# Kernel tuning notes

Measured on AMD Instinct MI355X. Metric: run time of the kernel, lower is better.

## Reference

```python
import jax, jax.numpy as jnp
import numpy as np


def _silu(x):
    return x * jax.nn.sigmoid(x)


def _ln(x, w, b, eps=1e-5):
    mu = x.mean(-1, keepdims=True)
    xc = x - mu
    var = (xc * xc).mean(-1, keepdims=True)
    return xc * jax.lax.rsqrt(var + eps) * w + b


def _segsum(a):
    # a: (..., Q) -> (..., Q, Q) lower-triangular cumulative segment sums
    Q = a.shape[-1]
    cs = jnp.cumsum(a, axis=-1)
    ss = cs[..., :, None] - cs[..., None, :]
    mask = jnp.tril(jnp.ones((Q, Q), dtype=bool))
    return jnp.where(mask, ss, -jnp.inf)


def _ssd(x, A, Bm, Cm, chunk=64):
    # Mamba2 SSD dual (chunked) form. x:(b,l,h,p) pre-scaled by dt, A:(b,l,h)=dt*A, Bm/Cm:(b,l,n)
    b, l, h, p = x.shape
    c = l // chunk
    x = x.reshape(b, c, chunk, h, p)
    A = A.reshape(b, c, chunk, h).transpose(0, 3, 1, 2)          # (b,h,c,q)
    Bm = Bm.reshape(b, c, chunk, -1)
    Cm = Cm.reshape(b, c, chunk, -1)
    Acs = jnp.cumsum(A, axis=-1)                                  # (b,h,c,q)
    Lmat = jnp.exp(_segsum(A))                                    # (b,h,c,q,q)
    Yd = jnp.einsum('bcln,bcsn,bhcls,bcshp->bclhp', Cm, Bm, Lmat, x)
    dec = jnp.exp(Acs[..., -1:] - Acs)                            # (b,h,c,q)
    states = jnp.einsum('bcln,bhcl,bclhp->bchpn', Bm, dec, x)     # (b,c,h,p,n)
    cdec = jnp.exp(Acs[..., -1]).transpose(2, 0, 1)               # (c,b,h)
    st = states.transpose(1, 0, 2, 3, 4)                          # (c,b,h,p,n)

    def step(carry, inp):
        s, d = inp
        return carry * d[..., None, None] + s, carry

    _, prev = jax.lax.scan(step, jnp.zeros_like(st[0]), (st, cdec))
    prev = prev.transpose(1, 0, 2, 3, 4)                          # (b,c,h,p,n)
    Yo = jnp.einsum('bcln,bchpn,bhcl->bclhp', Cm, prev, jnp.exp(Acs))
    return (Yd + Yo).reshape(b, l, h, p)


def _mamba(x, in_w, in_b, conv_w, conv_b, A_log, D, dt_bias, rms_w, out_w, headdim, d_state):
    b, l, _ = x.shape
    nh = A_log.shape[0]
    di = nh * headdim
    zxbcdt = x @ in_w.T + in_b
    z = zxbcdt[..., :di]
    xBC = zxbcdt[..., di:2 * di + 2 * d_state]
    dt = jax.nn.softplus(zxbcdt[..., -nh:] + dt_bias)             # (b,l,nh)
    K = conv_w.shape[-1]
    xp = jnp.pad(xBC, ((0, 0), (K - 1, 0), (0, 0)))               # causal depthwise conv
    xBC = sum(xp[:, k:k + l, :] * conv_w[:, k] for k in range(K))
    xBC = _silu(xBC + conv_b)
    xs = xBC[..., :di].reshape(b, l, nh, headdim)
    Bm = xBC[..., di:di + d_state]
    Cm = xBC[..., di + d_state:]
    A = -jnp.exp(A_log)
    y = _ssd(xs * dt[..., None], dt * A, Bm, Cm)
    y = y + D[None, None, :, None] * xs
    y = y.reshape(b, l, di) * _silu(z)                            # gated RMSNorm
    y = y * jax.lax.rsqrt(jnp.mean(y * y, -1, keepdims=True) + 1e-5) * rms_w
    return y @ out_w.T


def setup_inputs() -> dict:
    key = jax.random.key(0)
    ks = iter(jax.random.split(key, 64))

    def nrm(shape, s):
        return jax.random.normal(next(ks), shape, jnp.float32) * s

    d = {}
    d['x'] = jax.random.normal(next(ks), (4, 128, 64, 64), jnp.float32)
    d['seed_tok_w'] = nrm((8, 128), 0.08)
    d['seed_tok_b'] = jnp.zeros((8,), jnp.float32)
    d['seed_detok_w'] = nrm((128, 8), 0.3)
    d['seed_detok_b'] = jnp.zeros((128,), jnp.float32)
    d['sm_in_w'] = nrm((66, 8), 0.3)
    d['sm_in_b'] = jnp.zeros((66,), jnp.float32)
    d['sm_conv_w'] = nrm((48, 3), 0.3)
    d['sm_conv_b'] = jnp.zeros((48,), jnp.float32)
    d['sm_A_log'] = jnp.log(jnp.arange(1, 3, dtype=jnp.float32))
    d['sm_D'] = jnp.ones((2,), jnp.float32)
    d['sm_dt_bias'] = jnp.full((2,), -4.0, jnp.float32)
    d['sm_rms_w'] = jnp.ones((16,), jnp.float32)
    d['sm_out_w'] = nrm((8, 16), 0.2)
    d['cm_in_w'] = nrm((2, 196, 16), 0.2)
    d['cm_in_b'] = jnp.zeros((2, 196), jnp.float32)
    d['cm_conv_w'] = nrm((2, 160, 3), 0.3)
    d['cm_conv_b'] = jnp.zeros((2, 160), jnp.float32)
    d['cm_A_log'] = jnp.tile(jnp.log(jnp.arange(1, 5, dtype=jnp.float32)), (2, 1))
    d['cm_D'] = jnp.ones((2, 4), jnp.float32)
    d['cm_dt_bias'] = jnp.full((2, 4), -4.0, jnp.float32)
    d['cm_rms_w'] = jnp.ones((2, 32), jnp.float32)
    d['cm_out_w'] = nrm((2, 16, 32), 0.15)
    d['cross_W'] = jnp.eye(8, dtype=jnp.float32) + 0.01 * jax.random.normal(next(ks), (8, 8), jnp.float32)
    d['norm1_w'] = jnp.ones((128,), jnp.float32)
    d['norm1_b'] = jnp.zeros((128,), jnp.float32)
    d['norm2_w'] = jnp.ones((128,), jnp.float32)
    d['norm2_b'] = jnp.zeros((128,), jnp.float32)
    d['fc1_w'] = nrm((256, 128), 0.08)
    d['fc1_b'] = jnp.zeros((256,), jnp.float32)
    d['dw_w'] = nrm((256, 1, 3, 3), 0.2)
    d['dw_b'] = jnp.zeros((256,), jnp.float32)
    d['fc2_w'] = nrm((128, 256), 0.06)
    d['fc2_b'] = jnp.zeros((128,), jnp.float32)
    d['skip_scale'] = jnp.ones((1,), jnp.float32)
    return d


def reference(x, seed_tok_w, seed_tok_b, seed_detok_w, seed_detok_b,
              sm_in_w, sm_in_b, sm_conv_w, sm_conv_b, sm_A_log, sm_D, sm_dt_bias, sm_rms_w, sm_out_w,
              cm_in_w, cm_in_b, cm_conv_w, cm_conv_b, cm_A_log, cm_D, cm_dt_bias, cm_rms_w, cm_out_w,
              cross_W, norm1_w, norm1_b, norm2_w, norm2_b,
              fc1_w, fc1_b, dw_w, dw_b, fc2_w, fc2_b, skip_scale):
    B, C, H, W = x.shape
    L = H * W
    # --- GlobalSeed ---
    g = jnp.einsum('bchw,gc->bghw', x, seed_tok_w) + seed_tok_b[None, :, None, None]
    gf = g.reshape(B, -1, L).transpose(0, 2, 1)                   # (B,L,G)
    gf = _mamba(gf, sm_in_w, sm_in_b, sm_conv_w, sm_conv_b, sm_A_log, sm_D,
                sm_dt_bias, sm_rms_w, sm_out_w, 8, 16) + gf
    det = jnp.einsum('blg,cg->blc', gf, seed_detok_w) + seed_detok_b
    seed = x + det.transpose(0, 2, 1).reshape(B, C, H, W)
    # --- split-channel cascaded SSD (shared weights across splits) ---
    xn = _ln(x.reshape(B, C, L).transpose(0, 2, 1), norm1_w, norm1_b)   # (B,L,C)
    S = cross_W.shape[0]
    xs = jnp.stack(jnp.split(xn, S, axis=-1))                     # (S,B,L,C/S)

    def cascade(xi):
        for i in range(cm_in_w.shape[0]):
            xi = _mamba(xi, cm_in_w[i], cm_in_b[i], cm_conv_w[i], cm_conv_b[i],
                        cm_A_log[i], cm_D[i], cm_dt_bias[i], cm_rms_w[i], cm_out_w[i], 8, 64)
        return xi

    ys = jax.vmap(cascade)(xs) + xs * skip_scale
    # --- SubCrossToken mixing ---
    gm = ys.mean(axis=2)                                          # (S,B,Cs)
    wsm = jax.nn.softmax(cross_W, axis=1)
    gmix = jnp.einsum('qbc,qp->pbc', gm, wsm)
    ys = ys + gmix[:, :, None, :]
    out = ys.transpose(1, 2, 0, 3).reshape(B, L, -1)
    out = _ln(out, norm2_w, norm2_b)
    out = out.transpose(0, 2, 1).reshape(B, C, H, W) + seed
    # --- ConvFFN ---
    h1 = jnp.einsum('bchw,oc->bohw', out, fc1_w) + fc1_b[None, :, None, None]
    dw = jax.lax.conv_general_dilated(h1, dw_w, (1, 1), 'SAME',
                                      feature_group_count=h1.shape[1],
                                      dimension_numbers=('NCHW', 'OIHW', 'NCHW'))
    h2 = jax.nn.gelu(dw + dw_b[None, :, None, None])
    ffn = jnp.einsum('bohw,co->bchw', h2, fc2_w) + fc2_b[None, :, None, None]
    return out + ffn
```

## Files before the change

### kernel.cpp

```cpp
#include <hip/hip_runtime.h>
#include <math.h>

#define B_ 4
#define CCH 128
#define HH 64
#define WW 64
#define LL 4096
#define NCHK 64

__device__ __forceinline__ float siluf(float x) { return x / (1.f + __expf(-x)); }
__device__ __forceinline__ float softplusf(float x) { return (x > 20.f) ? x : log1pf(__expf(x)); }
__device__ __forceinline__ int swz(int n, int l) {
  return (n << 6) + ((((l >> 2) ^ ((n >> 2) & 15)) << 2) | (l & 3));
}

__global__ __launch_bounds__(256) void k_seedtok(const float* __restrict__ x,
    const float* __restrict__ w, const float* __restrict__ bias, float* __restrict__ gf)
{
  __shared__ float sw[8*128];
  int tid = threadIdx.x;
  for (int i = tid; i < 1024; i += 256) sw[i] = w[i];
  __syncthreads();
  int idx = blockIdx.x * 256 + tid;
  int b = idx / LL, l = idx % LL;
  const float* xp = x + (size_t)b*CCH*LL + l;
  float acc[8];
#pragma unroll
  for (int g = 0; g < 8; ++g) acc[g] = bias[g];
  for (int c = 0; c < CCH; ++c) {
    float xv = xp[(size_t)c*LL];
#pragma unroll
    for (int g = 0; g < 8; ++g) acc[g] += xv * sw[g*128 + c];
  }
  float* o = gf + (size_t)idx*8;
#pragma unroll
  for (int g = 0; g < 8; ++g) o[g] = acc[g];
}

template<int DIN, int NZ, int NDS, int NDT>
__global__ __launch_bounds__(256) void k_inproj(
    const float* __restrict__ src,
    const float* __restrict__ in_w, const float* __restrict__ in_b,
    const float* __restrict__ conv_w, const float* __restrict__ conv_b,
    const float* __restrict__ dt_bias,
    float* __restrict__ zb, float* __restrict__ dtb,
    float* __restrict__ xsb, float* __restrict__ Bb, float* __restrict__ Cb)
{
  constexpr int NXBC = NZ + 2*NDS;
  constexpr int NTOT = 2*NZ + 2*NDS + NDT;
  constexpr int NZQ  = NZ/4;
  constexpr int NDSQ = NDS/4;
  constexpr int XP   = DIN + 1;
  __shared__ float xt[66*XP];
  __shared__ float wl[NTOT*DIN];
  __shared__ float cwl[NXBC*3];
  __shared__ float cbl[NXBC];
  __shared__ float ibl[NTOT];
  __shared__ float dts[64*NDT];
  int tid = threadIdx.x;
  int seq = blockIdx.x >> 6;
  int l0  = (blockIdx.x & 63) << 6;
  for (int i = tid; i < NTOT*DIN; i += 256) wl[i] = in_w[i];
  for (int i = tid; i < NXBC*3; i += 256) cwl[i] = conv_w[i];
  for (int i = tid; i < NXBC; i += 256) cbl[i] = conv_b[i];
  for (int i = tid; i < NTOT; i += 256) ibl[i] = in_b[i];
  for (int i = tid; i < 66*DIN; i += 256) {
    int r = i / DIN, d = i % DIN;
    int l = l0 - 2 + r;
    xt[r*XP + d] = (l >= 0) ? src[((size_t)seq*LL + l)*DIN + d] : 0.f;
  }
  __syncthreads();
  int l = tid & 63, w = tid >> 6;
  float xr0[DIN], xr1[DIN], xr2[DIN];
#pragma unroll
  for (int d = 0; d < DIN; ++d) {
    xr0[d] = xt[l*XP + d];
    xr1[d] = xt[(l+1)*XP + d];
    xr2[d] = xt[(l+2)*XP + d];
  }
  size_t gl = (size_t)seq*LL + l0 + l;
  int tok = l0 + l;
  {
    float zv[NZQ];
#pragma unroll
    for (int j = 0; j < NZQ; ++j) {
      int row = w*NZQ + j;
      const float* wr = &wl[row*DIN];
      float acc = ibl[row];
#pragma unroll
      for (int d = 0; d < DIN; ++d) acc += xr2[d]*wr[d];
      zv[j] = acc;
    }
#pragma unroll
    for (int g = 0; g < NZQ/4; ++g)
      *(float4*)&zb[gl*NZ + w*NZQ + 4*g] = make_float4(zv[4*g], zv[4*g+1], zv[4*g+2], zv[4*g+3]);
  }
  if (w < NDT) {
    int row = NTOT - NDT + w;
    const float* wr = &wl[row*DIN];
    float acc = ibl[row] + dt_bias[w];
#pragma unroll
    for (int d = 0; d < DIN; ++d) acc += xr2[d]*wr[d];
    dts[l*NDT + w] = softplusf(acc);
  }
  float v0ok = (tok >= 2) ? 1.f : 0.f;
  float v1ok = (tok >= 1) ? 1.f : 0.f;
  {
    float xv[NZQ];
#pragma unroll
    for (int j = 0; j < NZQ; ++j) {
      int ch = w*NZQ + j;
      int row = NZ + ch;
      const float* wr = &wl[row*DIN];
      float p0 = 0.f, p1 = 0.f, p2 = 0.f;
#pragma unroll
      for (int d = 0; d < DIN; ++d) {
        float ww = wr[d];
        p0 += xr0[d]*ww; p1 += xr1[d]*ww; p2 += xr2[d]*ww;
      }
      float ib = ibl[row];
      float conv = cbl[ch] + (p0+ib)*v0ok*cwl[ch*3+0] + (p1+ib)*v1ok*cwl[ch*3+1] + (p2+ib)*cwl[ch*3+2];
      xv[j] = siluf(conv);
    }
#pragma unroll
    for (int g = 0; g < NZQ/4; ++g)
      *(float4*)&xsb[gl*NZ + w*NZQ + 4*g] = make_float4(xv[4*g], xv[4*g+1], xv[4*g+2], xv[4*g+3]);
  }
  {
    float bv[NDSQ];
#pragma unroll
    for (int j = 0; j < NDSQ; ++j) {
      int ch = NZ + w*NDSQ + j;
      int row = NZ + ch;
      const float* wr = &wl[row*DIN];
      float p0 = 0.f, p1 = 0.f, p2 = 0.f;
#pragma unroll
      for (int d = 0; d < DIN; ++d) {
        float ww = wr[d];
        p0 += xr0[d]*ww; p1 += xr1[d]*ww; p2 += xr2[d]*ww;
      }
      float ib = ibl[row];
      float conv = cbl[ch] + (p0+ib)*v0ok*cwl[ch*3+0] + (p1+ib)*v1ok*cwl[ch*3+1] + (p2+ib)*cwl[ch*3+2];
      bv[j] = siluf(conv);
    }
#pragma unroll
    for (int g = 0; g < NDSQ/4; ++g)
      *(float4*)&Bb[gl*NDS + w*NDSQ + 4*g] = make_float4(bv[4*g], bv[4*g+1], bv[4*g+2], bv[4*g+3]);
  }
  {
    float cv[NDSQ];
#pragma unroll
    for (int j = 0; j < NDSQ; ++j) {
      int ch = NZ + NDS + w*NDSQ + j;
      int row = NZ + ch;
      const float* wr = &wl[row*DIN];
      float p0 = 0.f, p1 = 0.f, p2 = 0.f;
#pragma unroll
      for (int d = 0; d < DIN; ++d) {
        float ww = wr[d];
        p0 += xr0[d]*ww; p1 += xr1[d]*ww; p2 += xr2[d]*ww;
      }
      float ib = ibl[row];
      float conv = cbl[ch] + (p0+ib)*v0ok*cwl[ch*3+0] + (p1+ib)*v1ok*cwl[ch*3+1] + (p2+ib)*cwl[ch*3+2];
      cv[j] = siluf(conv);
    }
#pragma unroll
    for (int g = 0; g < NDSQ/4; ++g)
      *(float4*)&Cb[gl*NDS + w*NDSQ + 4*g] = make_float4(cv[4*g], cv[4*g+1], cv[4*g+2], cv[4*g+3]);
  }
  __syncthreads();
  if (tid < 64) {
    if constexpr (NDT == 4) {
      float4 v = *(float4*)&dts[tid*4];
      *(float4*)&dtb[((size_t)seq*LL + l0 + tid)*4] = v;
    } else {
      float2 v = *(float2*)&dts[tid*NDT];
      *(float2*)&dtb[((size_t)seq*LL + l0 + tid)*NDT] = v;
    }
  }
}

template<int DS, int NH>
__global__ __launch_bounds__(256) void k_ssd1(
    const float* __restrict__ xs, const float* __restrict__ dtb,
    const float* __restrict__ Bb, const float* __restrict__ Cb,
    const float* __restrict__ A_log,
    float* __restrict__ ybuf, float* __restrict__ states,
    float* __restrict__ cdec, float* __restrict__ acsOut)
{
  constexpr int DI = NH*8;
  constexpr int NG = DS/4;
  __shared__ __align__(16) float BtBl[DS*64];
  __shared__ __align__(16) float CtGt[64*64];
  __shared__ __align__(16) float xde[NH*64*8];
  __shared__ __align__(16) float xde2[NH*64*8];
  int tid = threadIdx.x;
  int cid = blockIdx.x & 63;
  int seq = blockIdx.x >> 6;
  int l0  = cid << 6;
  for (int i = tid; i < 16*DS; i += 256) {
    int ng = i % NG, l = i / NG;
    size_t g = ((size_t)seq*LL + l0 + l)*DS + 4*ng;
    float4 bv = *(const float4*)&Bb[g];
    float4 cv = *(const float4*)&Cb[g];
    BtBl[swz(4*ng+0, l)] = bv.x; BtBl[swz(4*ng+1, l)] = bv.y;
    BtBl[swz(4*ng+2, l)] = bv.z; BtBl[swz(4*ng+3, l)] = bv.w;
    CtGt[swz(4*ng+0, l)] = cv.x; CtGt[swz(4*ng+1, l)] = cv.y;
    CtGt[swz(4*ng+2, l)] = cv.z; CtGt[swz(4*ng+3, l)] = cv.w;
  }
  __syncthreads();
  int lt = (tid >> 4) << 2, st = (tid & 15) << 2;
  float acc[4][4] = {};
#pragma unroll 4
  for (int n = 0; n < DS; ++n) {
    float4 cv = *(const float4*)&CtGt[swz(n, lt)];
    float4 bv = *(const float4*)&BtBl[swz(n, st)];
    float cc[4] = {cv.x, cv.y, cv.z, cv.w};
    float bb[4] = {bv.x, bv.y, bv.z, bv.w};
#pragma unroll
    for (int i2 = 0; i2 < 4; ++i2)
#pragma unroll
      for (int j2 = 0; j2 < 4; ++j2)
        acc[i2][j2] += cc[i2]*bb[j2];
  }
  __syncthreads();
#pragma unroll
  for (int j = 0; j < 4; ++j) {
    float4 gv = make_float4(acc[0][j], acc[1][j], acc[2][j], acc[3][j]);
    *(float4*)&CtGt[swz(st + j, lt)] = gv;
  }
  for (int i = tid; i < 16*DS; i += 256) {
    int ng = i % NG, l = i / NG;
    float4 bv = *(const float4*)&Bb[((size_t)seq*LL + l0 + l)*DS + 4*ng];
    *(float4*)&BtBl[l*DS + 4*ng] = bv;
  }
  __syncthreads();
  int w = tid >> 6, lane = tid & 63;
  if (w < NH) {
    int h = w;
    float dt_l = dtb[((size_t)seq*LL + l0 + lane)*NH + h];
    float Aval = -__expf(A_log[h]);
    float v = dt_l * Aval;
#pragma unroll
    for (int off = 1; off < 64; off <<= 1) {
      float t = __shfl_up(v, off, 64);
      if (lane >= off) v += t;
    }
    float acs_l = v;
    float m = __shfl(v, 31, 64);
    float acsLast = __shfl(v, 63, 64);
    float el = __expf(fminf(acs_l - m, 60.f));
    float fl = __expf(fminf(m - acs_l, 60.f));
    float dec = __expf(acsLast - acs_l);
    const float* xp = &xs[((size_t)seq*LL + l0 + lane)*DI + h*8];
    float4 x0 = *(const float4*)xp, x1 = *(const float4*)(xp + 4);
    float s1 = dt_l*fl, s2 = dt_l*dec;
    float* xe = &xde[(h*64 + lane)*8];
    float* xf = &xde2[(h*64 + lane)*8];
    *(float4*)xe     = make_float4(x0.x*s1, x0.y*s1, x0.z*s1, x0.w*s1);
    *(float4*)(xe+4) = make_float4(x1.x*s1, x1.y*s1, x1.z*s1, x1.w*s1);
// ... 102 lines not shown
    const float* __restrict__ ybuf, const float* __restrict__ zbuf,
    const float* __restrict__ rms_w, const float* __restrict__ out_w,
    float* __restrict__ dst, int resMode, const float* __restrict__ res,
    const float* __restrict__ skipPtr)
{
  __shared__ float ow[DOUT*DI];
  __shared__ float rw[DI];
  int tid = threadIdx.x;
  for (int i = tid; i < DOUT*DI; i += 256) ow[i] = out_w[i];
  for (int i = tid; i < DI; i += 256) rw[i] = rms_w[i];
  __syncthreads();
  size_t idx = (size_t)blockIdx.x*256 + tid;
  float y[DI];
  const float* yp = ybuf + idx*DI;
  const float* zp = zbuf + idx*DI;
  float ss = 0.f;
#pragma unroll
  for (int i = 0; i < DI; ++i) {
    float z = zp[i];
    float g = yp[i] * (z / (1.f + __expf(-z)));
    y[i] = g; ss += g*g;
  }
  float r = rsqrtf(ss*(1.f/DI) + 1e-5f);
#pragma unroll
  for (int i = 0; i < DI; ++i) y[i] *= r*rw[i];
  const float* rp = nullptr; float skip = 1.f;
  int seq = (int)(idx / LL), l = (int)(idx % LL);
  if (resMode == 1) rp = res + idx*DOUT;
  else if (resMode == 2) {
    int s = seq / B_, b = seq % B_;
    rp = res + ((size_t)b*LL + l)*CCH + s*DOUT;
    skip = skipPtr[0];
  }
  float* dp = dst + idx*DOUT;
#pragma unroll
  for (int o = 0; o < DOUT; ++o) {
    float acc = 0.f;
#pragma unroll
    for (int i = 0; i < DI; ++i) acc += y[i]*ow[o*DI + i];
    if (rp) acc += skip * rp[o];
    dp[o] = acc;
  }
}

__global__ __launch_bounds__(256) void k_detseed(const float* __restrict__ x,
    const float* __restrict__ gf2, const float* __restrict__ dw,
    const float* __restrict__ db, float* __restrict__ seed)
{
  size_t idx = (size_t)blockIdx.x*256 + threadIdx.x;
  int l = (int)(idx % LL); size_t t = idx / LL; int c = (int)(t % CCH); int b = (int)(t / CCH);
  const float* g = gf2 + ((size_t)b*LL + l)*8;
  float acc = db[c];
#pragma unroll
  for (int i = 0; i < 8; ++i) acc += g[i]*dw[c*8 + i];
  seed[idx] = x[idx] + acc;
}

__global__ __launch_bounds__(256) void k_ln1(const float* __restrict__ x,
    const float* __restrict__ w, const float* __restrict__ bb, float* __restrict__ xn)
{
  __shared__ float tile[128*65];
  __shared__ float mu[64], rs[64];
  int tid = threadIdx.x;
  int b = blockIdx.x >> 6;
  int l0 = (blockIdx.x & 63) << 6;
  for (int i = tid; i < 8192; i += 256) {
    int l = i & 63, c = i >> 6;
    tile[c*65 + l] = x[((size_t)b*CCH + c)*LL + l0 + l];
  }
  __syncthreads();
  if (tid < 64) {
    float s = 0.f;
    for (int c = 0; c < CCH; ++c) s += tile[c*65 + tid];
    float m = s * (1.f/CCH);
    float v = 0.f;
    for (int c = 0; c < CCH; ++c) { float d = tile[c*65 + tid] - m; v += d*d; }
    mu[tid] = m; rs[tid] = rsqrtf(v*(1.f/CCH) + 1e-5f);
  }
  __syncthreads();
  for (int i = tid; i < 8192; i += 256) {
    int c = i & 127, l = i >> 7;
    xn[((size_t)b*LL + l0 + l)*CCH + c] = (tile[c*65 + l] - mu[l])*rs[l]*w[c] + bb[c];
  }
}

__global__ __launch_bounds__(256) void k_split(const float* __restrict__ xn, float* __restrict__ X)
{
  size_t idx = (size_t)blockIdx.x*256 + threadIdx.x;
  int c = (int)(idx & 15); size_t t = idx >> 4; int l = (int)(t % LL); int seq = (int)(t / LL);
  int s = seq / B_, b = seq % B_;
  X[idx] = xn[((size_t)b*LL + l)*CCH + s*16 + c];
}

__global__ __launch_bounds__(256) void k_gm(const float* __restrict__ ys, float* __restrict__ gm)
{
  __shared__ float red[256];
  int tid = threadIdx.x;
  int seq = blockIdx.x;
  int c = tid & 15, lane = tid >> 4;
  float s = 0.f;
  for (int l = lane; l < LL; l += 16) s += ys[((size_t)seq*LL + l)*16 + c];
  red[tid] = s;
  __syncthreads();
  if (tid < 16) {
    float t = 0.f;
    for (int g = 0; g < 16; ++g) t += red[g*16 + tid];
    gm[(size_t)seq*16 + tid] = t * (1.f/LL);
  }
}

__global__ __launch_bounds__(256) void k_mix(const float* __restrict__ gm,
    const float* __restrict__ crossW, float* __restrict__ gmix)
{
  __shared__ float wsm[64];
  int tid = threadIdx.x;
  if (tid < 8) {
    float mx = -1e30f;
    for (int p = 0; p < 8; ++p) mx = fmaxf(mx, crossW[tid*8 + p]);
    float e[8]; float s = 0.f;
    for (int p = 0; p < 8; ++p) { e[p] = __expf(crossW[tid*8 + p] - mx); s += e[p]; }
    for (int p = 0; p < 8; ++p) wsm[tid*8 + p] = e[p] / s;
  }
  __syncthreads();
  for (int i = tid; i < 512; i += 256) {
    int c = i & 15; int bb = (i >> 4) & 3; int p = i >> 6;
    float acc = 0.f;
    for (int q = 0; q < 8; ++q) acc += gm[((size_t)(q*B_ + bb))*16 + c] * wsm[q*8 + p];
    gmix[((size_t)(p*B_ + bb))*16 + c] = acc;
  }
}

__global__ __launch_bounds__(256) void k_out2(const float* __restrict__ ys,
    const float* __restrict__ gmix, const float* __restrict__ w, const float* __restrict__ bb,
    const float* __restrict__ seed, float* __restrict__ outb)
{
  __shared__ float tile[128*65];
  __shared__ float mu[64], rs[64];
  int tid = threadIdx.x;
  int b = blockIdx.x >> 6;
  int l0 = (blockIdx.x & 63) << 6;
  for (int i = tid; i < 8192; i += 256) {
    int c = i & 15; int l = (i >> 4) & 63; int s = i >> 10;
    int seq = s*B_ + b;
    tile[(s*16 + c)*65 + l] = ys[((size_t)seq*LL + l0 + l)*16 + c] + gmix[(size_t)seq*16 + c];
  }
  __syncthreads();
  if (tid < 64) {
    float sm = 0.f;
    for (int c = 0; c < 128; ++c) sm += tile[c*65 + tid];
    float m = sm * (1.f/128.f);
    float v = 0.f;
    for (int c = 0; c < 128; ++c) { float d = tile[c*65 + tid] - m; v += d*d; }
    mu[tid] = m; rs[tid] = rsqrtf(v*(1.f/128.f) + 1e-5f);
  }
  __syncthreads();
  for (int i = tid; i < 8192; i += 256) {
    int l = i & 63, c = i >> 6;
    size_t gi = ((size_t)b*CCH + c)*LL + l0 + l;
    outb[gi] = (tile[c*65 + l] - mu[l])*rs[l]*w[c] + bb[c] + seed[gi];
  }
}

__global__ __launch_bounds__(256) void k_fc1(const float* __restrict__ src,
    const float* __restrict__ w, const float* __restrict__ bias, float* __restrict__ dst)
{
  constexpr int WP = 129;
  __shared__ float st[128*64];
  __shared__ float wt[64*WP];
  int tid = threadIdx.x;
  int blk = blockIdx.x;
  int ot = blk & 3;
  int lt = (blk >> 2) & 63;
  int b  = blk >> 8;
  int l0 = lt << 6, o0 = ot << 6;
// ... 81 lines not shown
      int l = i & 63, o = i >> 6;
      st[o*64 + l] = h2[((size_t)b*256 + ko + o)*LL + l0 + l];
    }
    __syncthreads();
#pragma unroll 4
    for (int o = 0; o < 128; ++o) {
      float4 sv = *(float4*)&st[o*64 + l4];
      float w0 = wt[(c2+0)*WP + ko + o];
      float w1 = wt[(c2+1)*WP + ko + o];
      a0[0] += w0*sv.x; a0[1] += w0*sv.y; a0[2] += w0*sv.z; a0[3] += w0*sv.w;
      a1[0] += w1*sv.x; a1[1] += w1*sv.y; a1[2] += w1*sv.z; a1[3] += w1*sv.w;
    }
  }
  float* rows[2] = {a0, a1};
#pragma unroll
  for (int j = 0; j < 2; ++j) {
    int c = c0 + c2 + j;
    float bi = bias[c];
    size_t gi = ((size_t)b*CCH + c)*LL + l0 + l4;
    float4 rv = *(const float4*)&resid[gi];
    float* a = rows[j];
    *(float4*)&dst[gi] = make_float4(a[0]+bi+rv.x, a[1]+bi+rv.y, a[2]+bi+rv.z, a[3]+bi+rv.w);
  }
}

extern "C" void kernel_launch(void* const* d_in, const int* in_sizes, int n_in,
                              void* d_out, int out_size, void* d_ws, size_t ws_size,
                              hipStream_t stream) {
  (void)in_sizes; (void)n_in; (void)out_size; (void)ws_size;
  const float* x        = (const float*)d_in[0];
  const float* tok_w    = (const float*)d_in[1];
  const float* tok_b    = (const float*)d_in[2];
  const float* detok_w  = (const float*)d_in[3];
  const float* detok_b  = (const float*)d_in[4];
  const float* sm_in_w  = (const float*)d_in[5];
  const float* sm_in_b  = (const float*)d_in[6];
  const float* sm_conv_w= (const float*)d_in[7];
  const float* sm_conv_b= (const float*)d_in[8];
  const float* sm_A_log = (const float*)d_in[9];
  const float* sm_D     = (const float*)d_in[10];
  const float* sm_dt_b  = (const float*)d_in[11];
  const float* sm_rms_w = (const float*)d_in[12];
  const float* sm_out_w = (const float*)d_in[13];
  const float* cm_in_w  = (const float*)d_in[14];
  const float* cm_in_b  = (const float*)d_in[15];
  const float* cm_conv_w= (const float*)d_in[16];
  const float* cm_conv_b= (const float*)d_in[17];
  const float* cm_A_log = (const float*)d_in[18];
  const float* cm_D     = (const float*)d_in[19];
  const float* cm_dt_b  = (const float*)d_in[20];
  const float* cm_rms_w = (const float*)d_in[21];
  const float* cm_out_w = (const float*)d_in[22];
  const float* cross_W  = (const float*)d_in[23];
  const float* n1w      = (const float*)d_in[24];
  const float* n1b      = (const float*)d_in[25];
  const float* n2w      = (const float*)d_in[26];
  const float* n2b      = (const float*)d_in[27];
  const float* fc1w     = (const float*)d_in[28];
  const float* fc1b     = (const float*)d_in[29];
  const float* dww      = (const float*)d_in[30];
  const float* dwb      = (const float*)d_in[31];
  const float* fc2w     = (const float*)d_in[32];
  const float* fc2b     = (const float*)d_in[33];
  const float* skp      = (const float*)d_in[34];
  float* ws  = (float*)d_ws;
  float* out = (float*)d_out;

  const size_t SEED = 0;
  const size_t XN   = 2097152;
  const size_t YS   = 4194304;
  const size_t OUTB = 6291456;
  const size_t GM   = 8388608;
  const size_t GMIX = 8389120;
  const size_t SCR  = 8389632;
  const size_t CZ   = SCR;
  const size_t CDT  = CZ   + 4194304;
  const size_t CXS  = CDT  + 524288;
  const size_t CBF  = CXS  + 4194304;
  const size_t CCF  = CBF  + 8388608;
  const size_t CACS = CCF  + 8388608;
  const size_t CST  = CACS + 2097152;
  const size_t CCD  = CST  + 4194304;
  const size_t CY   = CCD  + 8192;
  const size_t XA   = CY   + 4194304;
  const size_t XB   = XA   + 2097152;
  const size_t SGF  = SCR;
  const size_t SZ   = SCR + 131072;
  const size_t SDT  = SCR + 393216;
  const size_t SXS  = SCR + 425984;
  const size_t SB   = SCR + 688128;
  const size_t SC   = SCR + 950272;
  const size_t SACS = SCR + 1212416;
  const size_t SST  = SCR + 1245184;
  const size_t SCD  = SCR + 1310720;
  const size_t SY   = SCR + 1311232;
  const size_t SOUT = SCR + 1573376;
  const size_t H1 = SCR;
  const size_t H2 = SCR + 4194304;

  k_seedtok<<<64, 256, 0, stream>>>(x, tok_w, tok_b, ws + SGF);
  k_inproj<8,16,16,2><<<B_*64, 256, 0, stream>>>(ws + SGF, sm_in_w, sm_in_b, sm_conv_w,
      sm_conv_b, sm_dt_b, ws + SZ, ws + SDT, ws + SXS, ws + SB, ws + SC);
  k_ssd1<16,2><<<B_*NCHK, 256, 0, stream>>>(ws + SXS, ws + SDT, ws + SB, ws + SC,
      sm_A_log, ws + SY, ws + SST, ws + SCD, ws + SACS);
  k_scan<<<B_*2, 128, 0, stream>>>(ws + SST, ws + SCD, 128);
  k_ssd_yo<16,2><<<B_*NCHK, 256, 0, stream>>>(ws + SY, ws + SC, ws + SST, ws + SACS, sm_D, ws + SXS);
  k_gate<16,8><<<B_*LL/256, 256, 0, stream>>>(ws + SY, ws + SZ, sm_rms_w, sm_out_w,
      ws + SOUT, 1, ws + SGF, skp);
  k_detseed<<<B_*CCH*LL/256, 256, 0, stream>>>(x, ws + SOUT, detok_w, detok_b, ws + SEED);

  k_ln1<<<B_*64, 256, 0, stream>>>(x, n1w, n1b, ws + XN);
  k_split<<<32*LL*16/256, 256, 0, stream>>>(ws + XN, ws + XA);

  k_inproj<16,32,64,4><<<32*64, 256, 0, stream>>>(ws + XA, cm_in_w, cm_in_b, cm_conv_w,
      cm_conv_b, cm_dt_b, ws + CZ, ws + CDT, ws + CXS, ws + CBF, ws + CCF);
  k_ssd1<64,4><<<32*NCHK, 256, 0, stream>>>(ws + CXS, ws + CDT, ws + CBF, ws + CCF,
      cm_A_log, ws + CY, ws + CST, ws + CCD, ws + CACS);
  k_scan<<<32*4, 512, 0, stream>>>(ws + CST, ws + CCD, 512);
  k_ssd_yo<64,4><<<32*NCHK, 256, 0, stream>>>(ws + CY, ws + CCF, ws + CST, ws + CACS, cm_D, ws + CXS);
  k_gate<32,16><<<32*LL/256, 256, 0, stream>>>(ws + CY, ws + CZ, cm_rms_w, cm_out_w,
      ws + XB, 0, nullptr, skp);

  k_inproj<16,32,64,4><<<32*64, 256, 0, stream>>>(ws + XB, cm_in_w + 3136, cm_in_b + 196,
      cm_conv_w + 480, cm_conv_b + 160, cm_dt_b + 4, ws + CZ, ws + CDT, ws + CXS, ws + CBF, ws + CCF);
  k_ssd1<64,4><<<32*NCHK, 256, 0, stream>>>(ws + CXS, ws + CDT, ws + CBF, ws + CCF,
      cm_A_log + 4, ws + CY, ws + CST, ws + CCD, ws + CACS);
  k_scan<<<32*4, 512, 0, stream>>>(ws + CST, ws + CCD, 512);
  k_ssd_yo<64,4><<<32*NCHK, 256, 0, stream>>>(ws + CY, ws + CCF, ws + CST, ws + CACS, cm_D + 4, ws + CXS);
  k_gate<32,16><<<32*LL/256, 256, 0, stream>>>(ws + CY, ws + CZ, cm_rms_w + 32, cm_out_w + 512,
      ws + YS, 2, ws + XN, skp);

  k_gm<<<32, 256, 0, stream>>>(ws + YS, ws + GM);
  k_mix<<<1, 256, 0, stream>>>(ws + GM, cross_W, ws + GMIX);
  k_out2<<<B_*64, 256, 0, stream>>>(ws + YS, ws + GMIX, n2w, n2b, ws + SEED, ws + OUTB);

  k_fc1<<<B_*64*4, 256, 0, stream>>>(ws + OUTB, fc1w, fc1b, ws + H1);
  k_dw<<<B_*256*LL/256, 256, 0, stream>>>(ws + H1, dww, dwb, ws + H2);
  k_fc2<<<B_*64*4, 256, 0, stream>>>(ws + H2, fc2w, fc2b, ws + OUTB, out);
}
```

Before: 654.1 us.

## Register-tile in_proj over 4 tokens per thread and fuse split into it

Reworks the in_proj/conv kernel so each thread computes 4 consecutive tokens for a group of channels, keeping 6 input rows and one weight row in registers. Inputs are read straight from global memory as float4 instead of through a shared tile. Outputs are staged in padded shared tiles and written back with coalesced float4 stores. A srcMode flag lets the first cascade stage read the LN output through strides, which removes the separate k_split kernel and its round trip through global memory. The cost is higher register pressure from xr[6][DIN] and more shared memory for the output tiles, which may lower occupancy.

Measured after the change: 725.5 us. 1.11x slower.

```diff
diff --git a/kernel.cpp b/kernel.cpp
--- a/kernel.cpp
+++ b/kernel.cpp
@@ -39,7 +39,7 @@
 
 template<int DIN, int NZ, int NDS, int NDT>
 __global__ __launch_bounds__(256) void k_inproj(
-    const float* __restrict__ src,
+    const float* __restrict__ src, int srcMode,
     const float* __restrict__ in_w, const float* __restrict__ in_b,
     const float* __restrict__ conv_w, const float* __restrict__ conv_b,
     const float* __restrict__ dt_bias,
@@ -48,15 +48,20 @@
 {
   constexpr int NXBC = NZ + 2*NDS;
   constexpr int NTOT = 2*NZ + 2*NDS + NDT;
-  constexpr int NZQ  = NZ/4;
-  constexpr int NDSQ = NDS/4;
-  constexpr int XP   = DIN + 1;
-  __shared__ float xt[66*XP];
+  constexpr int ZR = NZ/16;
+  constexpr int BR = NDS/16;
+  constexpr int PZ = NZ + 1;
+  constexpr int PB = NDS + 1;
+  constexpr int PD = NDT + 1;
   __shared__ float wl[NTOT*DIN];
   __shared__ float cwl[NXBC*3];
   __shared__ float cbl[NXBC];
   __shared__ float ibl[NTOT];
-  __shared__ float dts[64*NDT];
+  __shared__ float zt[64*PZ];
+  __shared__ float xt2[64*PZ];
+  __shared__ float Bt[64*PB];
+  __shared__ float Ct[64*PB];
+  __shared__ float dtt[64*PD];
   int tid = threadIdx.x;
   int seq = blockIdx.x >> 6;
   int l0  = (blockIdx.x & 63) << 6;
@@ -64,118 +69,164 @@
   for (int i = tid; i < NXBC*3; i += 256) cwl[i] = conv_w[i];
   for (int i = tid; i < NXBC; i += 256) cbl[i] = conv_b[i];
   for (int i = tid; i < NTOT; i += 256) ibl[i] = in_b[i];
-  for (int i = tid; i < 66*DIN; i += 256) {
-    int r = i / DIN, d = i % DIN;
-    int l = l0 - 2 + r;
-    xt[r*XP + d] = (l >= 0) ? src[((size_t)seq*LL + l)*DIN + d] : 0.f;
-  }
-  __syncthreads();
-  int l = tid & 63, w = tid >> 6;
-  float xr0[DIN], xr1[DIN], xr2[DIN];
-#pragma unroll
-  for (int d = 0; d < DIN; ++d) {
-    xr0[d] = xt[l*XP + d];
-    xr1[d] = xt[(l+1)*XP + d];
-    xr2[d] = xt[(l+2)*XP + d];
-  }
-  size_t gl = (size_t)seq*LL + l0 + l;
-  int tok = l0 + l;
-  {
-    float zv[NZQ];
-#pragma unroll
-    for (int j = 0; j < NZQ; ++j) {
-      int row = w*NZQ + j;
-      const float* wr = &wl[row*DIN];
-      float acc = ibl[row];
-#pragma unroll
-      for (int d = 0; d < DIN; ++d) acc += xr2[d]*wr[d];
-      zv[j] = acc;
-    }
-#pragma unroll
-    for (int g = 0; g < NZQ/4; ++g)
-      *(float4*)&zb[gl*NZ + w*NZQ + 4*g] = make_float4(zv[4*g], zv[4*g+1], zv[4*g+2], zv[4*g+3]);
-  }
-  if (w < NDT) {
-    int row = NTOT - NDT + w;
-    const float* wr = &wl[row*DIN];
-    float acc = ibl[row] + dt_bias[w];
-#pragma unroll
-    for (int d = 0; d < DIN; ++d) acc += xr2[d]*wr[d];
-    dts[l*NDT + w] = softplusf(acc);
-  }
-  float v0ok = (tok >= 2) ? 1.f : 0.f;
-  float v1ok = (tok >= 1) ? 1.f : 0.f;
-  {
-    float xv[NZQ];
-#pragma unroll
-    for (int j = 0; j < NZQ; ++j) {
-      int ch = w*NZQ + j;
-      int row = NZ + ch;
-      const float* wr = &wl[row*DIN];
-      float p0 = 0.f, p1 = 0.f, p2 = 0.f;
+  __syncthreads();
+  int tg = tid & 15, cg = tid >> 4;
+  const float* sp; int sstr;
+  if (srcMode == 0) { sp = src + (size_t)seq*LL*DIN; sstr = DIN; }
+  else { sp = src + (size_t)(seq & 3)*LL*CCH + (seq >> 2)*16; sstr = CCH; }
+  float xr[6][DIN];
+#pragma unroll
+  for (int jj = 0; jj < 6; ++jj) {
+    int t = l0 + 4*tg - 2 + jj;
+    if (t >= 0) {
+      const float* p = sp + (size_t)t*sstr;
+#pragma unroll
+      for (int k = 0; k < DIN/4; ++k) {
+        float4 v = *(const float4*)(p + 4*k);
+        xr[jj][4*k+0]=v.x; xr[jj][4*k+1]=v.y; xr[jj][4*k+2]=v.z; xr[jj][4*k+3]=v.w;
+      }
+    } else {
+#pragma unroll
+      for (int d = 0; d < DIN; ++d) xr[jj][d] = 0.f;
+    }
+  }
+  float mk0[4], mk1[4];
+#pragma unroll
+  for (int j = 0; j < 4; ++j) {
+    int t = l0 + 4*tg + j;
+    mk0[j] = (t >= 2) ? 1.f : 0.f;
+    mk1[j] = (t >= 1) ? 1.f : 0.f;
+  }
+  float w[DIN];
+#pragma unroll
+  for (int r = 0; r < ZR; ++r) {
+    int row = cg*ZR + r;
+#pragma unroll
+    for (int k = 0; k < DIN/4; ++k) {
+      float4 v = *(const float4*)&wl[row*DIN + 4*k];
+      w[4*k]=v.x; w[4*k+1]=v.y; w[4*k+2]=v.z; w[4*k+3]=v.w;
+    }
+    float ib = ibl[row];
+#pragma unroll
+    for (int j = 0; j < 4; ++j) {
+      float acc = ib;
+#pragma unroll
+      for (int d = 0; d < DIN; ++d) acc += xr[2+j][d]*w[d];
+      zt[(4*tg+j)*PZ + row] = acc;
+    }
+  }
+  if (cg < NDT) {
+    int row = NTOT - NDT + cg;
+#pragma unroll
+    for (int k = 0; k < DIN/4; ++k) {
+      float4 v = *(const float4*)&wl[row*DIN + 4*k];
+      w[4*k]=v.x; w[4*k+1]=v.y; w[4*k+2]=v.z; w[4*k+3]=v.w;
+    }
+    float ib = ibl[row] + dt_bias[cg];
+#pragma unroll
+    for (int j = 0; j < 4; ++j) {
+      float acc = ib;
+#pragma unroll
+      for (int d = 0; d < DIN; ++d) acc += xr[2+j][d]*w[d];
+      dtt[(4*tg+j)*PD + cg] = softplusf(acc);
+    }
+  }
+#pragma unroll
+  for (int r = 0; r < ZR; ++r) {
+    int ch = cg*ZR + r;
+    int row = NZ + ch;
+#pragma unroll
+    for (int k = 0; k < DIN/4; ++k) {
+      float4 v = *(const float4*)&wl[row*DIN + 4*k];
+      w[4*k]=v.x; w[4*k+1]=v.y; w[4*k+2]=v.z; w[4*k+3]=v.w;
+    }
+    float ib = ibl[row];
+    float cw0 = cwl[ch*3+0], cw1 = cwl[ch*3+1], cw2 = cwl[ch*3+2], cb = cbl[ch];
+#pragma unroll
+    for (int j = 0; j < 4; ++j) {
+      float p0=0.f, p1=0.f, p2=0.f;
 #pragma unroll
       for (int d = 0; d < DIN; ++d) {
-        float ww = wr[d];
-        p0 += xr0[d]*ww; p1 += xr1[d]*ww; p2 += xr2[d]*ww;
+        p0 += xr[j][d]*w[d];
+        p1 += xr[j+1][d]*w[d];
+        p2 += xr[j+2][d]*w[d];
       }
-      float ib = ibl[row];
-      float conv = cbl[ch] + (p0+ib)*v0ok*cwl[ch*3+0] + (p1+ib)*v1ok*cwl[ch*3+1] + (p2+ib)*cwl[ch*3+2];
-      xv[j] = siluf(conv);
-    }
-#pragma unroll
-    for (int g = 0; g < NZQ/4; ++g)
-      *(float4*)&xsb[gl*NZ + w*NZQ + 4*g] = make_float4(xv[4*g], xv[4*g+1], xv[4*g+2], xv[4*g+3]);
-  }
-  {
-    float bv[NDSQ];
-#pragma unroll
-    for (int j = 0; j < NDSQ; ++j) {
-      int ch = NZ + w*NDSQ + j;
-      int row = NZ + ch;
-      const float* wr = &wl[row*DIN];
-      float p0 = 0.f, p1 = 0.f, p2 = 0.f;
+      float conv = cb + (p0+ib)*mk0[j]*cw0 + (p1+ib)*mk1[j]*cw1 + (p2+ib)*cw2;
+      xt2[(4*tg+j)*PZ + ch] = siluf(conv);
+    }
+  }
+#pragma unroll
+  for (int r = 0; r < BR; ++r) {
+    int chl = cg*BR + r;
+    int ch = NZ + chl;
+    int row = NZ + ch;
+#pragma unroll
+    for (int k = 0; k < DIN/4; ++k) {
+      float4 v = *(const float4*)&wl[row*DIN + 4*k];
+      w[4*k]=v.x; w[4*k+1]=v.y; w[4*k+2]=v.z; w[4*k+3]=v.w;
+    }
+    float ib = ibl[row];
+    float cw0 = cwl[ch*3+0], cw1 = cwl[ch*3+1], cw2 = cwl[ch*3+2], cb = cbl[ch];
+#pragma unroll
+    for (int j = 0; j < 4; ++j) {
+      float p0=0.f, p1=0.f, p2=0.f;
 #pragma unroll
       for (int d = 0; d < DIN; ++d) {
-        float ww = wr[d];
-        p0 += xr0[d]*ww; p1 += xr1[d]*ww; p2 += xr2[d]*ww;
+        p0 += xr[j][d]*w[d];
+        p1 += xr[j+1][d]*w[d];
+        p2 += xr[j+2][d]*w[d];
       }
-      float ib = ibl[row];
-      float conv = cbl[ch] + (p0+ib)*v0ok*cwl[ch*3+0] + (p1+ib)*v1ok*cwl[ch*3+1] + (p2+ib)*cwl[ch*3+2];
-      bv[j] = siluf(conv);
-    }
-#pragma unroll
-    for (int g = 0; g < NDSQ/4; ++g)
-      *(float4*)&Bb[gl*NDS + w*NDSQ + 4*g] = make_float4(bv[4*g], bv[4*g+1], bv[4*g+2], bv[4*g+3]);
-  }
-  {
-    float cv[NDSQ];
-#pragma unroll
-    for (int j = 0; j < NDSQ; ++j) {
-      int ch = NZ + NDS + w*NDSQ + j;
-      int row = NZ + ch;
-      const float* wr = &wl[row*DIN];
-      float p0 = 0.f, p1 = 0.f, p2 = 0.f;
+      float conv = cb + (p0+ib)*mk0[j]*cw0 + (p1+ib)*mk1[j]*cw1 + (p2+ib)*cw2;
+      Bt[(4*tg+j)*PB + chl] = siluf(conv);
+    }
+  }
+#pragma unroll
+  for (int r = 0; r < BR; ++r) {
+    int chl = cg*BR + r;
+    int ch = NZ + NDS + chl;
+    int row = NZ + ch;
+#pragma unroll
+    for (int k = 0; k < DIN/4; ++k) {
+      float4 v = *(const float4*)&wl[row*DIN + 4*k];
+      w[4*k]=v.x; w[4*k+1]=v.y; w[4*k+2]=v.z; w[4*k+3]=v.w;
+    }
+    float ib = ibl[row];
+    float cw0 = cwl[ch*3+0], cw1 = cwl[ch*3+1], cw2 = cwl[ch*3+2], cb = cbl[ch];
+#pragma unroll
+    for (int j = 0; j < 4; ++j) {
+      float p0=0.f, p1=0.f, p2=0.f;
 #pragma unroll
       for (int d = 0; d < DIN; ++d) {
-        float ww = wr[d];
-        p0 += xr0[d]*ww; p1 += xr1[d]*ww; p2 += xr2[d]*ww;
+        p0 += xr[j][d]*w[d];
+        p1 += xr[j+1][d]*w[d];
+        p2 += xr[j+2][d]*w[d];
       }
-      float ib = ibl[row];
-      float conv = cbl[ch] + (p0+ib)*v0ok*cwl[ch*3+0] + (p1+ib)*v1ok*cwl[ch*3+1] + (p2+ib)*cwl[ch*3+2];
-      cv[j] = siluf(conv);
-    }
-#pragma unroll
-    for (int g = 0; g < NDSQ/4; ++g)
-      *(float4*)&Cb[gl*NDS + w*NDSQ + 4*g] = make_float4(cv[4*g], cv[4*g+1], cv[4*g+2], cv[4*g+3]);
-  }
-  __syncthreads();
+      float conv = cb + (p0+ib)*mk0[j]*cw0 + (p1+ib)*mk1[j]*cw1 + (p2+ib)*cw2;
+      Ct[(4*tg+j)*PB + chl] = siluf(conv);
+    }
+  }
+  __syncthreads();
+  size_t gb = (size_t)seq*LL + l0;
+  for (int i = tid; i < 64*(NZ/4); i += 256) {
+    int l = i / (NZ/4), k = (i % (NZ/4))*4;
+    *(float4*)&zb[(gb+l)*NZ + k] =
+        make_float4(zt[l*PZ+k], zt[l*PZ+k+1], zt[l*PZ+k+2], zt[l*PZ+k+3]);
+    *(float4*)&xsb[(gb+l)*NZ + k] =
+        make_float4(xt2[l*PZ+k], xt2[l*PZ+k+1], xt2[l*PZ+k+2], xt2[l*PZ+k+3]);
+  }
+  for (int i = tid; i < 64*(NDS/4); i += 256) {
+    int l = i / (NDS/4), k = (i % (NDS/4))*4;
+    *(float4*)&Bb[(gb+l)*NDS + k] =
+        make_float4(Bt[l*PB+k], Bt[l*PB+k+1], Bt[l*PB+k+2], Bt[l*PB+k+3]);
+    *(float4*)&Cb[(gb+l)*NDS + k] =
+        make_float4(Ct[l*PB+k], Ct[l*PB+k+1], Ct[l*PB+k+2], Ct[l*PB+k+3]);
+  }
   if (tid < 64) {
     if constexpr (NDT == 4) {
-      float4 v = *(float4*)&dts[tid*4];
-      *(float4*)&dtb[((size_t)seq*LL + l0 + tid)*4] = v;
+      *(float4*)&dtb[(gb+tid)*4] =
+          make_float4(dtt[tid*PD], dtt[tid*PD+1], dtt[tid*PD+2], dtt[tid*PD+3]);
     } else {
-      float2 v = *(float2*)&dts[tid*NDT];
-      *(float2*)&dtb[((size_t)seq*LL + l0 + tid)*NDT] = v;
+      *(float2*)&dtb[(gb+tid)*NDT] = make_float2(dtt[tid*PD], dtt[tid*PD+1]);
     }
   }
 }
@@ -444,14 +495,6 @@
     int c = i & 127, l = i >> 7;
     xn[((size_t)b*LL + l0 + l)*CCH + c] = (tile[c*65 + l] - mu[l])*rs[l]*w[c] + bb[c];
   }
-}
-
-__global__ __launch_bounds__(256) void k_split(const float* __restrict__ xn, float* __restrict__ X)
-{
-  size_t idx = (size_t)blockIdx.x*256 + threadIdx.x;
-  int c = (int)(idx & 15); size_t t = idx >> 4; int l = (int)(t % LL); int seq = (int)(t / LL);
-  int s = seq / B_, b = seq % B_;
-  X[idx] = xn[((size_t)b*LL + l)*CCH + s*16 + c];
 }
 
 __global__ __launch_bounds__(256) void k_gm(const float* __restrict__ ys, float* __restrict__ gm)
@@ -716,7 +759,7 @@
   const size_t H2 = SCR + 4194304;
 
   k_seedtok<<<64, 256, 0, stream>>>(x, tok_w, tok_b, ws + SGF);
-  k_inproj<8,16,16,2><<<B_*64, 256, 0, stream>>>(ws + SGF, sm_in_w, sm_in_b, sm_conv_w,
+  k_inproj<8,16,16,2><<<B_*64, 256, 0, stream>>>(ws + SGF, 0, sm_in_w, sm_in_b, sm_conv_w,
       sm_conv_b, sm_dt_b, ws + SZ, ws + SDT, ws + SXS, ws + SB, ws + SC);
   k_ssd1<16,2><<<B_*NCHK, 256, 0, stream>>>(ws + SXS, ws + SDT, ws + SB, ws + SC,
       sm_A_log, ws + SY, ws + SST, ws + SCD, ws + SACS);
@@ -727,9 +770,8 @@
   k_detseed<<<B_*CCH*LL/256, 256, 0, stream>>>(x, ws + SOUT, detok_w, detok_b, ws + SEED);
 
   k_ln1<<<B_*64, 256, 0, stream>>>(x, n1w, n1b, ws + XN);
-  k_split<<<32*LL*16/256, 256, 0, stream>>>(ws + XN, ws + XA);
-
-  k_inproj<16,32,64,4><<<32*64, 256, 0, stream>>>(ws + XA, cm_in_w, cm_in_b, cm_conv_w,
+
+  k_inproj<16,32,64,4><<<32*64, 256, 0, stream>>>(ws + XN, 1, cm_in_w, cm_in_b, cm_conv_w,
       cm_conv_b, cm_dt_b, ws + CZ, ws + CDT, ws + CXS, ws + CBF, ws + CCF);
   k_ssd1<64,4><<<32*NCHK, 256, 0, stream>>>(ws + CXS, ws + CDT, ws + CBF, ws + CCF,
       cm_A_log, ws + CY, ws + CST, ws + CCD, ws + CACS);
@@ -738,7 +780,7 @@
   k_gate<32,16><<<32*LL/256, 256, 0, stream>>>(ws + CY, ws + CZ, cm_rms_w, cm_out_w,
       ws + XB, 0, nullptr, skp);
 
-  k_inproj<16,32,64,4><<<32*64, 256, 0, stream>>>(ws + XB, cm_in_w + 3136, cm_in_b + 196,
+  k_inproj<16,32,64,4><<<32*64, 256, 0, stream>>>(ws + XB, 0, cm_in_w + 3136, cm_in_b + 196,
       cm_conv_w + 480, cm_conv_b + 160, cm_dt_b + 4, ws + CZ, ws + CDT, ws + CXS, ws + CBF, ws + CCF);
   k_ssd1<64,4><<<32*NCHK, 256, 0, stream>>>(ws + CXS, ws + CDT, ws + CBF, ws + CCF,
       cm_A_log + 4, ws + CY, ws + CST, ws + CCD, ws + CACS);
```

## Fuse split into inproj strided loads and reuse conv projections via shuffles

Applied to the files above, without the earlier changes.

The separate k_split kernel is removed, and the first cross-Mamba in-projection now reads the layer-normed tensor directly with a channel stride and a per-sequence offset. Inside k_inproj, each lane computes its own token's xBC projection once. The two previous tokens' values now come from wavefront shuffles, with a small shared halo for the first two lanes, instead of three dot products per channel. This cuts one kernel launch, an 8 MB intermediate round trip, and about two thirds of the conv-path FMAs. The cost is strided global loads, an extra barrier and halo computation, and a reliance on 64-wide wavefronts for the shuffle.

Result: no change. 654.7 us (+0.1%).

```diff
diff --git a/kernel.cpp b/kernel.cpp
--- a/kernel.cpp
+++ b/kernel.cpp
@@ -39,7 +39,7 @@
 
 template<int DIN, int NZ, int NDS, int NDT>
 __global__ __launch_bounds__(256) void k_inproj(
-    const float* __restrict__ src,
+    const float* __restrict__ src, int srcMode,
     const float* __restrict__ in_w, const float* __restrict__ in_b,
     const float* __restrict__ conv_w, const float* __restrict__ conv_b,
     const float* __restrict__ dt_bias,
@@ -57,6 +57,7 @@
   __shared__ float cbl[NXBC];
   __shared__ float ibl[NTOT];
   __shared__ float dts[64*NDT];
+  __shared__ float hp[NXBC*2];
   int tid = threadIdx.x;
   int seq = blockIdx.x >> 6;
   int l0  = (blockIdx.x & 63) << 6;
@@ -64,118 +65,102 @@
   for (int i = tid; i < NXBC*3; i += 256) cwl[i] = conv_w[i];
   for (int i = tid; i < NXBC; i += 256) cbl[i] = conv_b[i];
   for (int i = tid; i < NTOT; i += 256) ibl[i] = in_b[i];
+  const float* sp; int sstr;
+  if (srcMode == 0) { sp = src + (size_t)seq*LL*DIN; sstr = DIN; }
+  else { sp = src + (size_t)(seq & 3)*LL*CCH + (seq >> 2)*16; sstr = CCH; }
   for (int i = tid; i < 66*DIN; i += 256) {
     int r = i / DIN, d = i % DIN;
     int l = l0 - 2 + r;
-    xt[r*XP + d] = (l >= 0) ? src[((size_t)seq*LL + l)*DIN + d] : 0.f;
-  }
-  __syncthreads();
-  int l = tid & 63, w = tid >> 6;
-  float xr0[DIN], xr1[DIN], xr2[DIN];
-#pragma unroll
-  for (int d = 0; d < DIN; ++d) {
-    xr0[d] = xt[l*XP + d];
-    xr1[d] = xt[(l+1)*XP + d];
-    xr2[d] = xt[(l+2)*XP + d];
-  }
+    xt[r*XP + d] = (l >= 0) ? sp[(size_t)l*sstr + d] : 0.f;
+  }
+  __syncthreads();
+  for (int i = tid; i < 2*NXBC; i += 256) {
+    int t = i & 1, ch = i >> 1;
+    const float* wr = &wl[(NZ + ch)*DIN];
+    const float* xp = &xt[t*XP];
+    float acc = 0.f;
+#pragma unroll
+    for (int d = 0; d < DIN; ++d) acc += xp[d]*wr[d];
+    hp[ch*2 + t] = acc;
+  }
+  __syncthreads();
+  int l = tid & 63, w4 = tid >> 6;
+  float xr2[DIN];
+#pragma unroll
+  for (int d = 0; d < DIN; ++d) xr2[d] = xt[(l+2)*XP + d];
   size_t gl = (size_t)seq*LL + l0 + l;
   int tok = l0 + l;
-  {
-    float zv[NZQ];
-#pragma unroll
-    for (int j = 0; j < NZQ; ++j) {
-      int row = w*NZQ + j;
-      const float* wr = &wl[row*DIN];
-      float acc = ibl[row];
-#pragma unroll
-      for (int d = 0; d < DIN; ++d) acc += xr2[d]*wr[d];
-      zv[j] = acc;
-    }
-#pragma unroll
-    for (int g = 0; g < NZQ/4; ++g)
-      *(float4*)&zb[gl*NZ + w*NZQ + 4*g] = make_float4(zv[4*g], zv[4*g+1], zv[4*g+2], zv[4*g+3]);
-  }
-  if (w < NDT) {
-    int row = NTOT - NDT + w;
-    const float* wr = &wl[row*DIN];
-    float acc = ibl[row] + dt_bias[w];
-#pragma unroll
-    for (int d = 0; d < DIN; ++d) acc += xr2[d]*wr[d];
-    dts[l*NDT + w] = softplusf(acc);
-  }
   float v0ok = (tok >= 2) ? 1.f : 0.f;
   float v1ok = (tok >= 1) ? 1.f : 0.f;
   {
+    float zv[NZQ];
+#pragma unroll
+    for (int j = 0; j < NZQ; ++j) {
+      int row = w4*NZQ + j;
+      const float* wr = &wl[row*DIN];
+      float acc = ibl[row];
+#pragma unroll
+      for (int d = 0; d < DIN; ++d) acc += xr2[d]*wr[d];
+      zv[j] = acc;
+    }
+#pragma unroll
+    for (int g = 0; g < NZQ/4; ++g)
+      *(float4*)&zb[gl*NZ + w4*NZQ + 4*g] = make_float4(zv[4*g], zv[4*g+1], zv[4*g+2], zv[4*g+3]);
+  }
+  if (w4 < NDT) {
+    int row = NTOT - NDT + w4;
+    const float* wr = &wl[row*DIN];
+    float acc = ibl[row] + dt_bias[w4];
+#pragma unroll
+    for (int d = 0; d < DIN; ++d) acc += xr2[d]*wr[d];
+    dts[l*NDT + w4] = softplusf(acc);
+  }
+  auto convch = [&](int ch) -> float {
+    int row = NZ + ch;
+    const float* wr = &wl[row*DIN];
+    float pm = 0.f;
+#pragma unroll
+    for (int d = 0; d < DIN; ++d) pm += xr2[d]*wr[d];
+    float m1 = __shfl_up(pm, 1, 64);
+    float m2 = __shfl_up(pm, 2, 64);
+    float h0 = hp[ch*2 + 0], h1 = hp[ch*2 + 1];
+    if (l == 0) m1 = h1;
+    m2 = (l == 0) ? h0 : ((l == 1) ? h1 : m2);
+    float ib = ibl[row];
+    float conv = cbl[ch] + (m2+ib)*v0ok*cwl[ch*3+0] + (m1+ib)*v1ok*cwl[ch*3+1] + (pm+ib)*cwl[ch*3+2];
+    return siluf(conv);
+  };
+  {
     float xv[NZQ];
 #pragma unroll
-    for (int j = 0; j < NZQ; ++j) {
-      int ch = w*NZQ + j;
-      int row = NZ + ch;
-      const float* wr = &wl[row*DIN];
-      float p0 = 0.f, p1 = 0.f, p2 = 0.f;
-#pragma unroll
-      for (int d = 0; d < DIN; ++d) {
-        float ww = wr[d];
-        p0 += xr0[d]*ww; p1 += xr1[d]*ww; p2 += xr2[d]*ww;
-      }
-      float ib = ibl[row];
-      float conv = cbl[ch] + (p0+ib)*v0ok*cwl[ch*3+0] + (p1+ib)*v1ok*cwl[ch*3+1] + (p2+ib)*cwl[ch*3+2];
-      xv[j] = siluf(conv);
-    }
+    for (int j = 0; j < NZQ; ++j) xv[j] = convch(w4*NZQ + j);
 #pragma unroll
     for (int g = 0; g < NZQ/4; ++g)
-      *(float4*)&xsb[gl*NZ + w*NZQ + 4*g] = make_float4(xv[4*g], xv[4*g+1], xv[4*g+2], xv[4*g+3]);
+      *(float4*)&xsb[gl*NZ + w4*NZQ + 4*g] = make_float4(xv[4*g], xv[4*g+1], xv[4*g+2], xv[4*g+3]);
   }
   {
     float bv[NDSQ];
 #pragma unroll
-    for (int j = 0; j < NDSQ; ++j) {
-      int ch = NZ + w*NDSQ + j;
-      int row = NZ + ch;
-      const float* wr = &wl[row*DIN];
-      float p0 = 0.f, p1 = 0.f, p2 = 0.f;
-#pragma unroll
-      for (int d = 0; d < DIN; ++d) {
-        float ww = wr[d];
-        p0 += xr0[d]*ww; p1 += xr1[d]*ww; p2 += xr2[d]*ww;
-      }
-      float ib = ibl[row];
-      float conv = cbl[ch] + (p0+ib)*v0ok*cwl[ch*3+0] + (p1+ib)*v1ok*cwl[ch*3+1] + (p2+ib)*cwl[ch*3+2];
-      bv[j] = siluf(conv);
-    }
+    for (int j = 0; j < NDSQ; ++j) bv[j] = convch(NZ + w4*NDSQ + j);
 #pragma unroll
     for (int g = 0; g < NDSQ/4; ++g)
-      *(float4*)&Bb[gl*NDS + w*NDSQ + 4*g] = make_float4(bv[4*g], bv[4*g+1], bv[4*g+2], bv[4*g+3]);
+      *(float4*)&Bb[gl*NDS + w4*NDSQ + 4*g] = make_float4(bv[4*g], bv[4*g+1], bv[4*g+2], bv[4*g+3]);
   }
   {
     float cv[NDSQ];
 #pragma unroll
-    for (int j = 0; j < NDSQ; ++j) {
-      int ch = NZ + NDS + w*NDSQ + j;
-      int row = NZ + ch;
-      const float* wr = &wl[row*DIN];
-      float p0 = 0.f, p1 = 0.f, p2 = 0.f;
-#pragma unroll
-      for (int d = 0; d < DIN; ++d) {
-        float ww = wr[d];
-        p0 += xr0[d]*ww; p1 += xr1[d]*ww; p2 += xr2[d]*ww;
-      }
-      float ib = ibl[row];
-      float conv = cbl[ch] + (p0+ib)*v0ok*cwl[ch*3+0] + (p1+ib)*v1ok*cwl[ch*3+1] + (p2+ib)*cwl[ch*3+2];
-      cv[j] = siluf(conv);
-    }
+    for (int j = 0; j < NDSQ; ++j) cv[j] = convch(NZ + NDS + w4*NDSQ + j);
 #pragma unroll
     for (int g = 0; g < NDSQ/4; ++g)
-      *(float4*)&Cb[gl*NDS + w*NDSQ + 4*g] = make_float4(cv[4*g], cv[4*g+1], cv[4*g+2], cv[4*g+3]);
+      *(float4*)&Cb[gl*NDS + w4*NDSQ + 4*g] = make_float4(cv[4*g], cv[4*g+1], cv[4*g+2], cv[4*g+3]);
   }
   __syncthreads();
   if (tid < 64) {
     if constexpr (NDT == 4) {
-      float4 v = *(float4*)&dts[tid*4];
-      *(float4*)&dtb[((size_t)seq*LL + l0 + tid)*4] = v;
+      *(float4*)&dtb[((size_t)seq*LL + l0 + tid)*4] =
+          make_float4(dts[tid*4], dts[tid*4+1], dts[tid*4+2], dts[tid*4+3]);
     } else {
-      float2 v = *(float2*)&dts[tid*NDT];
-      *(float2*)&dtb[((size_t)seq*LL + l0 + tid)*NDT] = v;
+      *(float2*)&dtb[((size_t)seq*LL + l0 + tid)*NDT] = make_float2(dts[tid*NDT], dts[tid*NDT+1]);
     }
   }
 }
@@ -444,14 +429,6 @@
     int c = i & 127, l = i >> 7;
     xn[((size_t)b*LL + l0 + l)*CCH + c] = (tile[c*65 + l] - mu[l])*rs[l]*w[c] + bb[c];
   }
-}
-
-__global__ __launch_bounds__(256) void k_split(const float* __restrict__ xn, float* __restrict__ X)
-{
-  size_t idx = (size_t)blockIdx.x*256 + threadIdx.x;
-  int c = (int)(idx & 15); size_t t = idx >> 4; int l = (int)(t % LL); int seq = (int)(t / LL);
-  int s = seq / B_, b = seq % B_;
-  X[idx] = xn[((size_t)b*LL + l)*CCH + s*16 + c];
 }
 
 __global__ __launch_bounds__(256) void k_gm(const float* __restrict__ ys, float* __restrict__ gm)
@@ -699,8 +676,7 @@
   const size_t CST  = CACS + 2097152;
   const size_t CCD  = CST  + 4194304;
   const size_t CY   = CCD  + 8192;
-  const size_t XA   = CY   + 4194304;
-  const size_t XB   = XA   + 2097152;
+  const size_t XB   = CY   + 4194304;
   const size_t SGF  = SCR;
   const size_t SZ   = SCR + 131072;
   const size_t SDT  = SCR + 393216;
@@ -716,7 +692,7 @@
   const size_t H2 = SCR + 4194304;
 
   k_seedtok<<<64, 256, 0, stream>>>(x, tok_w, tok_b, ws + SGF);
-  k_inproj<8,16,16,2><<<B_*64, 256, 0, stream>>>(ws + SGF, sm_in_w, sm_in_b, sm_conv_w,
+  k_inproj<8,16,16,2><<<B_*64, 256, 0, stream>>>(ws + SGF, 0, sm_in_w, sm_in_b, sm_conv_w,
       sm_conv_b, sm_dt_b, ws + SZ, ws + SDT, ws + SXS, ws + SB, ws + SC);
   k_ssd1<16,2><<<B_*NCHK, 256, 0, stream>>>(ws + SXS, ws + SDT, ws + SB, ws + SC,
       sm_A_log, ws + SY, ws + SST, ws + SCD, ws + SACS);
@@ -727,9 +703,8 @@
   k_detseed<<<B_*CCH*LL/256, 256, 0, stream>>>(x, ws + SOUT, detok_w, detok_b, ws + SEED);
 
   k_ln1<<<B_*64, 256, 0, stream>>>(x, n1w, n1b, ws + XN);
-  k_split<<<32*LL*16/256, 256, 0, stream>>>(ws + XN, ws + XA);
-
-  k_inproj<16,32,64,4><<<32*64, 256, 0, stream>>>(ws + XA, cm_in_w, cm_in_b, cm_conv_w,
+
+  k_inproj<16,32,64,4><<<32*64, 256, 0, stream>>>(ws + XN, 1, cm_in_w, cm_in_b, cm_conv_w,
       cm_conv_b, cm_dt_b, ws + CZ, ws + CDT, ws + CXS, ws + CBF, ws + CCF);
   k_ssd1<64,4><<<32*NCHK, 256, 0, stream>>>(ws + CXS, ws + CDT, ws + CBF, ws + CCF,
       cm_A_log, ws + CY, ws + CST, ws + CCD, ws + CACS);
@@ -738,7 +713,7 @@
   k_gate<32,16><<<32*LL/256, 256, 0, stream>>>(ws + CY, ws + CZ, cm_rms_w, cm_out_w,
       ws + XB, 0, nullptr, skp);
 
-  k_inproj<16,32,64,4><<<32*64, 256, 0, stream>>>(ws + XB, cm_in_w + 3136, cm_in_b + 196,
+  k_inproj<16,32,64,4><<<32*64, 256, 0, stream>>>(ws + XB, 0, cm_in_w + 3136, cm_in_b + 196,
       cm_conv_w + 480, cm_conv_b + 160, cm_dt_b + 4, ws + CZ, ws + CDT, ws + CXS, ws + CBF, ws + CCF);
   k_ssd1<64,4><<<32*NCHK, 256, 0, stream>>>(ws + CXS, ws + CDT, ws + CBF, ws + CCF,
       cm_A_log + 4, ws + CY, ws + CST, ws + CCD, ws + CACS);
```
